# Kernel tuning notes

Hardware: AMD Instinct MI355X
Metric: run time of the kernel (lower is better)

## Reference

```python
import jax, jax.numpy as jnp
import numpy as np

B, C, H, W = 4, 128, 64, 64
CO = 128

def setup_inputs() -> dict:
    key = jax.random.key(0)
    ks = jax.random.split(key, 10)
    s = 1.0 / np.sqrt(C)
    return {
        "x":  jax.random.normal(ks[0], (B, C, H, W), dtype=jnp.float32),
        "Wq": jax.random.uniform(ks[1], (C, C), jnp.float32, -s, s),
        "bq": jax.random.uniform(ks[2], (C,), jnp.float32, -s, s),
        "Wk": jax.random.uniform(ks[3], (C, C), jnp.float32, -s, s),
        "bk": jax.random.uniform(ks[4], (C,), jnp.float32, -s, s),
        "Wv": jax.random.uniform(ks[5], (C, C), jnp.float32, -s, s),
        "bv": jax.random.uniform(ks[6], (C,), jnp.float32, -s, s),
        "gamma": jnp.ones((1,), dtype=jnp.float32),
        "Wo": jax.random.uniform(ks[7], (CO, C), jnp.float32, -s, s),
        "bo": jax.random.uniform(ks[8], (CO,), jnp.float32, -s, s),
    }

def reference(x, Wq, bq, Wk, bk, Wv, bv, gamma, Wo, bo):
    b, c, h, w = x.shape
    xf = x.reshape(b, c, h * w)                       # [B,C,N]
    # 1x1 convs == channel matmuls
    Q = jnp.einsum('oc,bcn->bon', Wq, xf) + bq[None, :, None]
    K = jnp.einsum('oc,bcn->bon', Wk, xf) + bk[None, :, None]
    V = jnp.einsum('oc,bcn->bon', Wv, xf) + bv[None, :, None]
    # attention[b,i,j] = softmax_j( sum_c Q[b,c,i] K[b,c,j] )  (unscaled)
    scores = jnp.einsum('bci,bcj->bij', Q, K)         # [B,N,N]
    attn = jax.nn.softmax(scores, axis=-1)
    # selfAtten[b,c,i] = sum_j V[b,c,j] attn[b,i,j]
    sa = jnp.einsum('bcj,bij->bci', V, attn)          # [B,C,N]
    sa = gamma[0] * sa + xf
    out = jnp.einsum('oc,bcn->bon', Wo, sa) + bo[None, :, None]
    return out.reshape(b, Wo.shape[0], h, w)
```

## Files before the change

### kernel.cpp

```cpp
#include <hip/hip_runtime.h>

#define BB 4
#define CC 128
#define NN 4096

typedef float f32x4 __attribute__((ext_vector_type(4)));
typedef __bf16 bf16x8 __attribute__((ext_vector_type(8)));

#define MFMA16(A, B, C) __builtin_amdgcn_mfma_f32_16x16x32_bf16((A), (B), (C), 0, 0, 0)

typedef __attribute__((address_space(3))) void lds_void;
typedef __attribute__((address_space(1))) void glob_void;
#define GLD16(g, l) __builtin_amdgcn_global_load_lds((const glob_void*)(g), (lds_void*)(l), 16, 0, 0)

__device__ __forceinline__ int fK(int r) { return (r & 3) | (((r >> 3) & 1) << 2); }

__global__ __launch_bounds__(256)
void pack_w(const float* __restrict__ Wq, const float* __restrict__ bq,
            const float* __restrict__ Wk, const float* __restrict__ bk,
            const float* __restrict__ Wv, const float* __restrict__ bv,
            const float* __restrict__ Wo, const float* __restrict__ bo,
            __bf16* __restrict__ Wpk, float* __restrict__ bpk)
{
    const int mat = blockIdx.x >> 3;
    const int p   = blockIdx.x & 7;
    const int tid = threadIdx.x;
    const int ks  = tid >> 6;
    const int lane = tid & 63;
    const int col = lane & 15;
    const int quad = lane >> 4;

    const float LOG2E = 1.44269504088896340736f;
    const float* W = (mat == 0) ? Wq : (mat == 1) ? Wk : (mat == 2) ? Wv : Wo;
    const float* bsrc = (mat == 0) ? bq : (mat == 1) ? bk : (mat == 2) ? bv : bo;
    const float scale = (mat == 0) ? LOG2E : 1.0f;

    const float* wr = W + (size_t)(p * 16 + col) * CC + ks * 32 + quad * 8;
    float4 f0 = *(const float4*)wr;
    float4 f1 = *(const float4*)(wr + 4);
    bf16x8 a;
    a[0]=(__bf16)(f0.x*scale); a[1]=(__bf16)(f0.y*scale);
    a[2]=(__bf16)(f0.z*scale); a[3]=(__bf16)(f0.w*scale);
    a[4]=(__bf16)(f1.x*scale); a[5]=(__bf16)(f1.y*scale);
    a[6]=(__bf16)(f1.z*scale); a[7]=(__bf16)(f1.w*scale);
    *(bf16x8*)&Wpk[(((size_t)(mat * 8 + p) * 4 + ks) * 64 + lane) * 8] = a;

    if (p == 0 && tid < 128) bpk[mat * 128 + tid] = bsrc[tid] * scale;
}

__global__ __launch_bounds__(256, 2)
void qkv_gemm(const float* __restrict__ x,
              const __bf16* __restrict__ Wpk, const float* __restrict__ bpk,
              __bf16* __restrict__ Qt, __bf16* __restrict__ Kt,
              __bf16* __restrict__ Vblk)
{
    const int b    = blockIdx.y;
    const int n0   = blockIdx.x * 64;
    const int tid  = threadIdx.x;
    const int lane = tid & 63;
    const int wv   = __builtin_amdgcn_readfirstlane(tid >> 6);
    const int col  = lane & 15;
    const int quad = lane >> 4;

    __shared__ __bf16 xs[64 * 144];
    __shared__ __bf16 vs[128 * 64];

    {
        const int n  = tid & 63;
        const int c0 = tid >> 6;
        const float* xb = x + ((size_t)b * CC) * NN + n0 + n;
#pragma unroll
        for (int i = 0; i < 16; i++) {
            int c = (c0 + i * 4) * 2;
            float v0 = xb[(size_t)c * NN];
            float v1 = xb[(size_t)(c + 1) * NN];
            union { __bf16 h[2]; unsigned u; } pk;
            pk.h[0] = (__bf16)v0; pk.h[1] = (__bf16)v1;
            *(unsigned*)&xs[n * 144 + c] = pk.u;
        }
    }
    __syncthreads();

    bf16x8 Bf[4][4];
#pragma unroll
    for (int ng = 0; ng < 4; ng++)
#pragma unroll
        for (int ks = 0; ks < 4; ks++)
            Bf[ng][ks] = *(const bf16x8*)&xs[(ng * 16 + col) * 144 + ks * 32 + quad * 8];

#pragma unroll 1
    for (int p = 0; p < 6; p++) {
        const int mat = p >> 1;
        const int pg  = wv + 4 * (p & 1);
        const int o0  = pg * 16;

        bf16x8 Af[4];
#pragma unroll
        for (int ks = 0; ks < 4; ks++)
            Af[ks] = *(const bf16x8*)&Wpk[(((size_t)(mat * 8 + pg) * 4 + ks) * 64 + lane) * 8];

        f32x4 D[4];
#pragma unroll
        for (int ng = 0; ng < 4; ng++) D[ng] = (f32x4){0.f, 0.f, 0.f, 0.f};
#pragma unroll
        for (int ks = 0; ks < 4; ks++)
#pragma unroll
            for (int ng = 0; ng < 4; ng++)
                D[ng] = MFMA16(Af[ks], Bf[ng][ks], D[ng]);

        float4 bias = *(const float4*)(bpk + mat * 128 + o0 + quad * 4);

#pragma unroll
        for (int ng = 0; ng < 4; ng++) {
            const int n = ng * 16 + col;
            float v[4];
#pragma unroll
            for (int r = 0; r < 4; r++)
                v[r] = D[ng][r] + ((const float*)&bias)[r];
            if (mat == 0) {
                union { __bf16 h[4]; uint2 u; } pk;
                for (int r = 0; r < 4; r++) pk.h[r] = (__bf16)v[r];
                *(uint2*)&Qt[((size_t)b * NN + n0 + n) * CC + o0 + quad * 4] = pk.u;
            } else if (mat == 1) {
                const int chunk = ((o0 + quad * 4) >> 3) ^ fK(n);
                union { __bf16 h[4]; uint2 u; } pk;
                for (int r = 0; r < 4; r++) pk.h[r] = (__bf16)v[r];
                *(uint2*)&Kt[((size_t)b * NN + n0 + n) * CC + chunk * 8 + (quad & 1) * 4] = pk.u;
            } else {
#pragma unroll
                for (int r = 0; r < 4; r++)
                    vs[(o0 + quad * 4 + r) * 64 + n] = (__bf16)v[r];
            }
        }
    }
    __syncthreads();

    {
        __bf16* vd = Vblk + (((size_t)b * 64 + (n0 >> 6)) * CC) * 64;
#pragma unroll
        for (int e = 0; e < 4; e++) {
            int idx = e * 256 + tid;
            int c = idx >> 3, ch = idx & 7;
            bf16x8 v = *(const bf16x8*)&vs[c * 64 + ch * 8];
            *(bf16x8*)&vd[c * 64 + ((ch ^ (c & 7)) * 8)] = v;
        }
    }
}

__global__ __launch_bounds__(256, 2)
void flash_attn(const __bf16* __restrict__ Qt, const __bf16* __restrict__ Kt,
                const __bf16* __restrict__ Vblk,
                float* __restrict__ Opart, float* __restrict__ Lpart)
{
    const int blk = blockIdx.x;
    const int b   = blk & 3;
    const int jhi = (blk >> 2) & 1;
    const int rr  = blk >> 3;
    const int js  = jhi * 2 + (rr & 1);
    const int i0  = (rr >> 1) * 128;

    const int tid  = threadIdx.x;
    const int lane = tid & 63;
    const int iw   = __builtin_amdgcn_readfirstlane(tid >> 6);
    const int col  = lane & 15;
    const int quad = lane >> 4;

    __shared__ __align__(16) char smem[69632];
    char* Kbytes = smem;
    char* Vbytes = smem + 16384;
    __bf16* Vh = (__bf16*)Vbytes;

#pragma unroll
    for (int e = 0; e < 4; e++) {
        int k = e * 256 + tid;
        Vh[128 * 64 + k] = (__bf16)((k < 64) ? 1.0f : 0.0f);
    }

    const __bf16* Qb = Qt + (size_t)b * NN * CC;
    const char*   Ks = (const char*)(Kt + (size_t)b * NN * CC);
    const char*   Vs = (const char*)(Vblk + ((size_t)b * 64 * CC) * 64);

    const int ibase = i0 + iw * 32;

    bf16x8 qf[2][4];
#pragma unroll
    for (int ig = 0; ig < 2; ig++)
#pragma unroll
        for (int ks = 0; ks < 4; ks++)
            qf[ig][ks] = *(const bf16x8*)(Qb + (size_t)(ibase + ig * 16 + col) * CC
                                             + ks * 32 + quad * 8);

    const int perm = ((col & 12) << 1) | (col & 3);
    const int fR   = fK(perm);
    int kaddr[4][4];
    const int joff[4] = {0, 4, 32, 36};
#pragma unroll
    for (int jg = 0; jg < 4; jg++)
#pragma unroll
        for (int ks = 0; ks < 4; ks++)
            kaddr[jg][ks] = (perm + joff[jg]) * 256 + (((ks * 4 + quad) ^ fR) * 16);
    int vaddr[8][2], oaddr[2];
#pragma unroll
    for (int cg = 0; cg < 8; cg++)
#pragma unroll
        for (int t = 0; t < 2; t++)
            vaddr[cg][t] = (cg * 16 + col) * 128 + (((t * 4 + quad) ^ (col & 7)) * 16);
#pragma unroll
    for (int t = 0; t < 2; t++)
        oaddr[t] = (128 + col) * 128 + (t * 4 + quad) * 16;

    f32x4 O[2][8], lacc[2];
#pragma unroll
    for (int ig = 0; ig < 2; ig++) {
#pragma unroll
        for (int cg = 0; cg < 8; cg++) O[ig][cg] = (f32x4){0.f, 0.f, 0.f, 0.f};
        lacc[ig] = (f32x4){0.f, 0.f, 0.f, 0.f};
    }

#pragma unroll 1
    for (int t16 = 0; t16 < 16; t16++) {
        const int jt = js * 16 + t16;
        const char* kg = Ks + (size_t)jt * 16384;
        const char* vg = Vs + (size_t)jt * 16384;
#pragma unroll
        for (int q = 0; q < 4; q++) {
            const int call = iw * 4 + q;
            GLD16(kg + call * 1024 + lane * 16, Kbytes + call * 1024 + lane * 16);
            GLD16(vg + call * 1024 + lane * 16, Vbytes + call * 1024 + lane * 16);
        }
        __syncthreads();

        f32x4 S[2][4];
#pragma unroll
        for (int ig = 0; ig < 2; ig++)
#pragma unroll
            for (int jg = 0; jg < 4; jg++)
                S[ig][jg] = (f32x4){-32.f, -32.f, -32.f, -32.f};
#pragma unroll
        for (int ks = 0; ks < 4; ks++) {
            bf16x8 k0 = *(const bf16x8*)(Kbytes + kaddr[0][ks]);
            bf16x8 k1 = *(const bf16x8*)(Kbytes + kaddr[1][ks]);
            bf16x8 k2 = *(const bf16x8*)(Kbytes + kaddr[2][ks]);
            bf16x8 k3 = *(const bf16x8*)(Kbytes + kaddr[3][ks]);
            S[0][0] = MFMA16(k0, qf[0][ks], S[0][0]);
            S[1][0] = MFMA16(k0, qf[1][ks], S[1][0]);
            S[0][1] = MFMA16(k1, qf[0][ks], S[0][1]);
            S[1][1] = MFMA16(k1, qf[1][ks], S[1][1]);
            S[0][2] = MFMA16(k2, qf[0][ks], S[0][2]);
            S[1][2] = MFMA16(k2, qf[1][ks], S[1][2]);
            S[0][3] = MFMA16(k3, qf[0][ks], S[0][3]);
            S[1][3] = MFMA16(k3, qf[1][ks], S[1][3]);
        }

#pragma unroll
        for (int ig = 0; ig < 2; ig++)
#pragma unroll
            for (int jg = 0; jg < 4; jg++)
#pragma unroll
                for (int r = 0; r < 4; r++)
                    S[ig][jg][r] = __builtin_amdgcn_exp2f(S[ig][jg][r]);

#pragma unroll
        for (int t = 0; t < 2; t++) {
            bf16x8 pf0, pf1;
#pragma unroll
            for (int e = 0; e < 8; e++) {
                int jg = 2 * t + (e >> 2), r = e & 3;
                pf0[e] = (__bf16)S[0][jg][r];
                pf1[e] = (__bf16)S[1][jg][r];
            }
#pragma unroll
            for (int cg = 0; cg < 8; cg++) {
                bf16x8 vf = *(const bf16x8*)(Vbytes + vaddr[cg][t]);
                O[0][cg] = MFMA16(vf, pf0, O[0][cg]);
                O[1][cg] = MFMA16(vf, pf1, O[1][cg]);
            }
            bf16x8 of = *(const bf16x8*)(Vbytes + oaddr[t]);
            lacc[0] = MFMA16(of, pf0, lacc[0]);
            lacc[1] = MFMA16(of, pf1, lacc[1]);
        }
        __syncthreads();
    }

    float* Ol = (float*)smem;
    float* Ll = (float*)(smem + 67584);
#pragma unroll
    for (int ig = 0; ig < 2; ig++) {
#pragma unroll
        for (int cg = 0; cg < 8; cg++)
#pragma unroll
            for (int r = 0; r < 4; r++)
                Ol[(cg * 16 + quad * 4 + r) * 132 + iw * 32 + ig * 16 + col] = O[ig][cg][r];
        if (quad == 0) Ll[iw * 32 + ig * 16 + col] = lacc[ig][0];
    }
    __syncthreads();
    {
        float* Od = Opart + (((size_t)b * 4 + js) * CC) * NN + i0;
#pragma unroll
        for (int e = 0; e < 16; e++) {
            int k = e * 256 + tid;
            int c = k >> 5, i4 = (k & 31) * 4;
            float4 v = *(const float4*)(Ol + c * 132 + i4);
            *(float4*)(Od + (size_t)c * NN + i4) = v;
        }
        if (tid < 128)
            Lpart[((size_t)b * 4 + js) * NN + i0 + tid] = Ll[tid];
    }
}

__global__ __launch_bounds__(256, 2)
void proj_out(const float* __restrict__ Opart, const float* __restrict__ Lpart,
              const float* __restrict__ x,
              const __bf16* __restrict__ Wpk, const float* __restrict__ bpk,
              const float* __restrict__ gamma, float* __restrict__ out)
{
    const int b    = blockIdx.y;
    const int n0   = blockIdx.x * 64;
    const int tid  = threadIdx.x;
    const int lane = tid & 63;
    const int wv   = __builtin_amdgcn_readfirstlane(tid >> 6);
    const int col  = lane & 15;
    const int quad = lane >> 4;

    __shared__ __bf16 sas[64 * 144];
    __shared__ float  outs[128 * 66];

    const float g = gamma[0];

    {
        const int n  = tid & 63;
        const int c0 = tid >> 6;
        const size_t nb = (size_t)b * 4;
        float l = Lpart[(nb + 0) * NN + n0 + n] + Lpart[(nb + 1) * NN + n0 + n]
                + Lpart[(nb + 2) * NN + n0 + n] + Lpart[(nb + 3) * NN + n0 + n];
        const float gl = g / l;
        const float* xb = x + ((size_t)b * CC) * NN + n0 + n;
        const float* Ob = Opart + (nb * CC) * NN + n0 + n;
#pragma unroll
        for (int i = 0; i < 16; i++) {
            int c = (c0 + i * 4) * 2;
            float s0 = 0.f, s1 = 0.f;
#pragma unroll
            for (int jsp = 0; jsp < 4; jsp++) {
                s0 += Ob[((size_t)jsp * CC + c) * NN];
                s1 += Ob[((size_t)jsp * CC + c + 1) * NN];
            }
            float v0 = xb[(size_t)c * NN] + s0 * gl;
            float v1 = xb[(size_t)(c + 1) * NN] + s1 * gl;
            union { __bf16 h[2]; unsigned u; } pk;
            pk.h[0] = (__bf16)v0; pk.h[1] = (__bf16)v1;
            *(unsigned*)&sas[n * 144 + c] = pk.u;
        }
    }
    __syncthreads();

    bf16x8 Bf[4][4];
#pragma unroll
    for (int ng = 0; ng < 4; ng++)
#pragma unroll
        for (int ks = 0; ks < 4; ks++)
            Bf[ng][ks] = *(const bf16x8*)&sas[(ng * 16 + col) * 144 + ks * 32 + quad * 8];

#pragma unroll
    for (int p = 0; p < 2; p++) {
        const int pg = wv * 2 + p;
        const int o0 = pg * 16;
        bf16x8 Af[4];
#pragma unroll
        for (int ks = 0; ks < 4; ks++)
            Af[ks] = *(const bf16x8*)&Wpk[(((size_t)(3 * 8 + pg) * 4 + ks) * 64 + lane) * 8];

        f32x4 D[4];
#pragma unroll
        for (int ng = 0; ng < 4; ng++) D[ng] = (f32x4){0.f, 0.f, 0.f, 0.f};
#pragma unroll
        for (int ks = 0; ks < 4; ks++)
#pragma unroll
            for (int ng = 0; ng < 4; ng++)
                D[ng] = MFMA16(Af[ks], Bf[ng][ks], D[ng]);

        float4 bias = *(const float4*)(bpk + 3 * 128 + o0 + quad * 4);
#pragma unroll
        for (int ng = 0; ng < 4; ng++)
#pragma unroll
            for (int r = 0; r < 4; r++)
                outs[(o0 + quad * 4 + r) * 66 + ng * 16 + col]
                    = D[ng][r] + ((const float*)&bias)[r];
    }
    __syncthreads();

    {
        float* od = out + ((size_t)b * CC) * NN + n0;
#pragma unroll
        for (int e = 0; e < 32; e++) {
            int k = e * 256 + tid;
            int o = k >> 6, n = k & 63;
            od[(size_t)o * NN + n] = outs[o * 66 + n];
        }
    }
}

extern "C" void kernel_launch(void* const* d_in, const int* in_sizes, int n_in,
                              void* d_out, int out_size, void* d_ws, size_t ws_size,
                              hipStream_t stream)
{
    const float* x  = (const float*)d_in[0];
    const float* Wq = (const float*)d_in[1];
    const float* bq = (const float*)d_in[2];
    const float* Wk = (const float*)d_in[3];
    const float* bk = (const float*)d_in[4];
    const float* Wv = (const float*)d_in[5];
    const float* bv = (const float*)d_in[6];
    const float* gm = (const float*)d_in[7];
    const float* Wo = (const float*)d_in[8];
    const float* bo = (const float*)d_in[9];

    __bf16* Qt    = (__bf16*)d_ws;
    __bf16* Kt    = Qt + (size_t)BB * NN * CC;
    __bf16* Vblk  = Kt + (size_t)BB * NN * CC;
    float*  Opart = (float*)(Vblk + (size_t)BB * NN * CC);
    float*  Lpart = Opart + (size_t)16 * CC * NN;
    __bf16* Wpk   = (__bf16*)(Lpart + (size_t)16 * NN);
    float*  bpk   = (float*)(Wpk + 4 * 8 * 4 * 64 * 8);
    float*  out   = (float*)d_out;

    pack_w<<<32, 256, 0, stream>>>(Wq, bq, Wk, bk, Wv, bv, Wo, bo, Wpk, bpk);
    qkv_gemm<<<dim3(64, 4), 256, 0, stream>>>(x, Wpk, bpk, Qt, Kt, Vblk);
    flash_attn<<<512, 256, 0, stream>>>(Qt, Kt, Vblk, Opart, Lpart);
    proj_out<<<dim3(64, 4), 256, 0, stream>>>(Opart, Lpart, x, Wpk, bpk, gm, out);
}
```

Baseline: 132.3 us.

## Double key-split factor and halve GEMM tiles to raise parallelism

Flash attention now splits the key dimension into 8 partitions instead of 4, launching 1024 blocks with half the key tiles each. Its shared memory drops to about 34 KB and launch bounds are raised to 3 blocks per CU. Partial outputs are written directly to global memory rather than staged through LDS, and the QKV and output-projection kernels use 32-column tiles to double their grid sizes. The aim is better CU occupancy and load balance, at the cost of twice the partial-output traffic and more reduction work in proj_out.

```diff
diff --git a/kernel.cpp b/kernel.cpp
--- a/kernel.cpp
+++ b/kernel.cpp
@@ -55,23 +55,23 @@
               __bf16* __restrict__ Vblk)
 {
     const int b    = blockIdx.y;
-    const int n0   = blockIdx.x * 64;
+    const int n0   = blockIdx.x * 32;
     const int tid  = threadIdx.x;
     const int lane = tid & 63;
     const int wv   = __builtin_amdgcn_readfirstlane(tid >> 6);
     const int col  = lane & 15;
     const int quad = lane >> 4;
 
-    __shared__ __bf16 xs[64 * 144];
-    __shared__ __bf16 vs[128 * 64];
+    __shared__ __bf16 xs[32 * 144];
+    __shared__ __bf16 vs[128 * 32];
 
     {
-        const int n  = tid & 63;
-        const int c0 = tid >> 6;
+        const int n  = tid & 31;
+        const int c0 = tid >> 5;
         const float* xb = x + ((size_t)b * CC) * NN + n0 + n;
 #pragma unroll
-        for (int i = 0; i < 16; i++) {
-            int c = (c0 + i * 4) * 2;
+        for (int i = 0; i < 8; i++) {
+            int c = (c0 + i * 8) * 2;
             float v0 = xb[(size_t)c * NN];
             float v1 = xb[(size_t)(c + 1) * NN];
             union { __bf16 h[2]; unsigned u; } pk;
@@ -81,9 +81,9 @@
     }
     __syncthreads();
 
-    bf16x8 Bf[4][4];
-#pragma unroll
-    for (int ng = 0; ng < 4; ng++)
+    bf16x8 Bf[2][4];
+#pragma unroll
+    for (int ng = 0; ng < 2; ng++)
 #pragma unroll
         for (int ks = 0; ks < 4; ks++)
             Bf[ng][ks] = *(const bf16x8*)&xs[(ng * 16 + col) * 144 + ks * 32 + quad * 8];
@@ -99,19 +99,19 @@
         for (int ks = 0; ks < 4; ks++)
             Af[ks] = *(const bf16x8*)&Wpk[(((size_t)(mat * 8 + pg) * 4 + ks) * 64 + lane) * 8];
 
-        f32x4 D[4];
-#pragma unroll
-        for (int ng = 0; ng < 4; ng++) D[ng] = (f32x4){0.f, 0.f, 0.f, 0.f};
-#pragma unroll
-        for (int ks = 0; ks < 4; ks++)
-#pragma unroll
-            for (int ng = 0; ng < 4; ng++)
+        f32x4 D[2];
+#pragma unroll
+        for (int ng = 0; ng < 2; ng++) D[ng] = (f32x4){0.f, 0.f, 0.f, 0.f};
+#pragma unroll
+        for (int ks = 0; ks < 4; ks++)
+#pragma unroll
+            for (int ng = 0; ng < 2; ng++)
                 D[ng] = MFMA16(Af[ks], Bf[ng][ks], D[ng]);
 
         float4 bias = *(const float4*)(bpk + mat * 128 + o0 + quad * 4);
 
 #pragma unroll
-        for (int ng = 0; ng < 4; ng++) {
+        for (int ng = 0; ng < 2; ng++) {
             const int n = ng * 16 + col;
             float v[4];
 #pragma unroll
@@ -122,14 +122,15 @@
                 for (int r = 0; r < 4; r++) pk.h[r] = (__bf16)v[r];
                 *(uint2*)&Qt[((size_t)b * NN + n0 + n) * CC + o0 + quad * 4] = pk.u;
             } else if (mat == 1) {
-                const int chunk = ((o0 + quad * 4) >> 3) ^ fK(n);
+                const int rin = ((n0 & 32) + n) & 63;
+                const int chunk = ((o0 + quad * 4) >> 3) ^ fK(rin);
                 union { __bf16 h[4]; uint2 u; } pk;
                 for (int r = 0; r < 4; r++) pk.h[r] = (__bf16)v[r];
                 *(uint2*)&Kt[((size_t)b * NN + n0 + n) * CC + chunk * 8 + (quad & 1) * 4] = pk.u;
             } else {
 #pragma unroll
                 for (int r = 0; r < 4; r++)
-                    vs[(o0 + quad * 4 + r) * 64 + n] = (__bf16)v[r];
+                    vs[(o0 + quad * 4 + r) * 32 + n] = (__bf16)v[r];
             }
         }
     }
@@ -137,27 +138,29 @@
 
     {
         __bf16* vd = Vblk + (((size_t)b * 64 + (n0 >> 6)) * CC) * 64;
-#pragma unroll
-        for (int e = 0; e < 4; e++) {
+        const int chbase = (n0 & 32) >> 3;
+#pragma unroll
+        for (int e = 0; e < 2; e++) {
             int idx = e * 256 + tid;
-            int c = idx >> 3, ch = idx & 7;
-            bf16x8 v = *(const bf16x8*)&vs[c * 64 + ch * 8];
-            *(bf16x8*)&vd[c * 64 + ((ch ^ (c & 7)) * 8)] = v;
+            int c = idx >> 2, chl = idx & 3;
+            bf16x8 v = *(const bf16x8*)&vs[c * 32 + chl * 8];
+            *(bf16x8*)&vd[c * 64 + (((chbase + chl) ^ (c & 7)) * 8)] = v;
         }
     }
 }
 
-__global__ __launch_bounds__(256, 2)
+__global__ __launch_bounds__(256, 3)
 void flash_attn(const __bf16* __restrict__ Qt, const __bf16* __restrict__ Kt,
                 const __bf16* __restrict__ Vblk,
                 float* __restrict__ Opart, float* __restrict__ Lpart)
 {
     const int blk = blockIdx.x;
-    const int b   = blk & 3;
-    const int jhi = (blk >> 2) & 1;
-    const int rr  = blk >> 3;
-    const int js  = jhi * 2 + (rr & 1);
-    const int i0  = (rr >> 1) * 128;
+    const int b    = blk & 3;
+    const int jlow = (blk >> 2) & 1;
+    const int jhigh = (blk >> 3) & 3;
+    const int it32  = blk >> 5;
+    const int js   = (jhigh << 1) | jlow;
+    const int i0   = it32 * 128;
 
     const int tid  = threadIdx.x;
     const int lane = tid & 63;
@@ -165,7 +168,7 @@
     const int col  = lane & 15;
     const int quad = lane >> 4;
 
-    __shared__ __align__(16) char smem[69632];
+    __shared__ __align__(16) char smem[34816];
     char* Kbytes = smem;
     char* Vbytes = smem + 16384;
     __bf16* Vh = (__bf16*)Vbytes;
@@ -218,8 +221,8 @@
     }
 
 #pragma unroll 1
-    for (int t16 = 0; t16 < 16; t16++) {
-        const int jt = js * 16 + t16;
+    for (int t8 = 0; t8 < 8; t8++) {
+        const int jt = js * 8 + t8;
         const char* kg = Ks + (size_t)jt * 16384;
         const char* vg = Vs + (size_t)jt * 16384;
 #pragma unroll
@@ -282,29 +285,22 @@
         __syncthreads();
     }
 
-    float* Ol = (float*)smem;
-    float* Ll = (float*)(smem + 67584);
-#pragma unroll
-    for (int ig = 0; ig < 2; ig++) {
-#pragma unroll
-        for (int cg = 0; cg < 8; cg++)
-#pragma unroll
-            for (int r = 0; r < 4; r++)
-                Ol[(cg * 16 + quad * 4 + r) * 132 + iw * 32 + ig * 16 + col] = O[ig][cg][r];
-        if (quad == 0) Ll[iw * 32 + ig * 16 + col] = lacc[ig][0];
-    }
-    __syncthreads();
     {
-        float* Od = Opart + (((size_t)b * 4 + js) * CC) * NN + i0;
-#pragma unroll
-        for (int e = 0; e < 16; e++) {
-            int k = e * 256 + tid;
-            int c = k >> 5, i4 = (k & 31) * 4;
-            float4 v = *(const float4*)(Ol + c * 132 + i4);
-            *(float4*)(Od + (size_t)c * NN + i4) = v;
-        }
-        if (tid < 128)
-            Lpart[((size_t)b * 4 + js) * NN + i0 + tid] = Ll[tid];
+        float* Od = Opart + (((size_t)b * 8 + js) * CC) * NN + ibase;
+#pragma unroll
+        for (int ig = 0; ig < 2; ig++)
+#pragma unroll
+            for (int cg = 0; cg < 8; cg++)
+#pragma unroll
+                for (int r = 0; r < 4; r++)
+                    Od[(size_t)(cg * 16 + quad * 4 + r) * NN + ig * 16 + col]
+                        = O[ig][cg][r];
+        if (quad == 0) {
+            float* Ld = Lpart + ((size_t)b * 8 + js) * NN + ibase;
+#pragma unroll
+            for (int ig = 0; ig < 2; ig++)
+                Ld[ig * 16 + col] = lacc[ig][0];
+        }
     }
 }
 
@@ -315,33 +311,35 @@
               const float* __restrict__ gamma, float* __restrict__ out)
 {
     const int b    = blockIdx.y;
-    const int n0   = blockIdx.x * 64;
+    const int n0   = blockIdx.x * 32;
     const int tid  = threadIdx.x;
     const int lane = tid & 63;
     const int wv   = __builtin_amdgcn_readfirstlane(tid >> 6);
     const int col  = lane & 15;
     const int quad = lane >> 4;
 
-    __shared__ __bf16 sas[64 * 144];
-    __shared__ float  outs[128 * 66];
+    __shared__ __bf16 sas[32 * 144];
+    __shared__ float  outs[128 * 34];
 
     const float g = gamma[0];
 
     {
-        const int n  = tid & 63;
-        const int c0 = tid >> 6;
-        const size_t nb = (size_t)b * 4;
-        float l = Lpart[(nb + 0) * NN + n0 + n] + Lpart[(nb + 1) * NN + n0 + n]
-                + Lpart[(nb + 2) * NN + n0 + n] + Lpart[(nb + 3) * NN + n0 + n];
+        const int n  = tid & 31;
+        const int c0 = tid >> 5;
+        const size_t nb = (size_t)b * 8;
+        float l = 0.f;
+#pragma unroll
+        for (int jsp = 0; jsp < 8; jsp++)
+            l += Lpart[(nb + jsp) * NN + n0 + n];
         const float gl = g / l;
         const float* xb = x + ((size_t)b * CC) * NN + n0 + n;
         const float* Ob = Opart + (nb * CC) * NN + n0 + n;
 #pragma unroll
-        for (int i = 0; i < 16; i++) {
-            int c = (c0 + i * 4) * 2;
+        for (int i = 0; i < 8; i++) {
+            int c = (c0 + i * 8) * 2;
             float s0 = 0.f, s1 = 0.f;
 #pragma unroll
-            for (int jsp = 0; jsp < 4; jsp++) {
+            for (int jsp = 0; jsp < 8; jsp++) {
                 s0 += Ob[((size_t)jsp * CC + c) * NN];
                 s1 += Ob[((size_t)jsp * CC + c + 1) * NN];
             }
@@ -354,9 +352,9 @@
     }
     __syncthreads();
 
-    bf16x8 Bf[4][4];
-#pragma unroll
-    for (int ng = 0; ng < 4; ng++)
+    bf16x8 Bf[2][4];
+#pragma unroll
+    for (int ng = 0; ng < 2; ng++)
 #pragma unroll
         for (int ks = 0; ks < 4; ks++)
             Bf[ng][ks] = *(const bf16x8*)&sas[(ng * 16 + col) * 144 + ks * 32 + quad * 8];
@@ -370,21 +368,21 @@
         for (int ks = 0; ks < 4; ks++)
             Af[ks] = *(const bf16x8*)&Wpk[(((size_t)(3 * 8 + pg) * 4 + ks) * 64 + lane) * 8];
 
-        f32x4 D[4];
-#pragma unroll
-        for (int ng = 0; ng < 4; ng++) D[ng] = (f32x4){0.f, 0.f, 0.f, 0.f};
-#pragma unroll
-        for (int ks = 0; ks < 4; ks++)
-#pragma unroll
-            for (int ng = 0; ng < 4; ng++)
+        f32x4 D[2];
+#pragma unroll
+        for (int ng = 0; ng < 2; ng++) D[ng] = (f32x4){0.f, 0.f, 0.f, 0.f};
+#pragma unroll
+        for (int ks = 0; ks < 4; ks++)
+#pragma unroll
+            for (int ng = 0; ng < 2; ng++)
                 D[ng] = MFMA16(Af[ks], Bf[ng][ks], D[ng]);
 
         float4 bias = *(const float4*)(bpk + 3 * 128 + o0 + quad * 4);
 #pragma unroll
-        for (int ng = 0; ng < 4; ng++)
+        for (int ng = 0; ng < 2; ng++)
 #pragma unroll
             for (int r = 0; r < 4; r++)
-                outs[(o0 + quad * 4 + r) * 66 + ng * 16 + col]
+                outs[(o0 + quad * 4 + r) * 34 + ng * 16 + col]
                     = D[ng][r] + ((const float*)&bias)[r];
     }
     __syncthreads();
@@ -392,10 +390,10 @@
     {
         float* od = out + ((size_t)b * CC) * NN + n0;
 #pragma unroll
-        for (int e = 0; e < 32; e++) {
+        for (int e = 0; e < 16; e++) {
             int k = e * 256 + tid;
-            int o = k >> 6, n = k & 63;
-            od[(size_t)o * NN + n] = outs[o * 66 + n];
+            int o = k >> 5, n = k & 31;
+            od[(size_t)o * NN + n] = outs[o * 34 + n];
         }
     }
 }
@@ -419,13 +417,13 @@
     __bf16* Kt    = Qt + (size_t)BB * NN * CC;
     __bf16* Vblk  = Kt + (size_t)BB * NN * CC;
     float*  Opart = (float*)(Vblk + (size_t)BB * NN * CC);
-    float*  Lpart = Opart + (size_t)16 * CC * NN;
-    __bf16* Wpk   = (__bf16*)(Lpart + (size_t)16 * NN);
+    float*  Lpart = Opart + (size_t)32 * CC * NN;
+    __bf16* Wpk   = (__bf16*)(Lpart + (size_t)32 * NN);
     float*  bpk   = (float*)(Wpk + 4 * 8 * 4 * 64 * 8);
     float*  out   = (float*)d_out;
 
     pack_w<<<32, 256, 0, stream>>>(Wq, bq, Wk, bk, Wv, bv, Wo, bo, Wpk, bpk);
-    qkv_gemm<<<dim3(64, 4), 256, 0, stream>>>(x, Wpk, bpk, Qt, Kt, Vblk);
-    flash_attn<<<512, 256, 0, stream>>>(Qt, Kt, Vblk, Opart, Lpart);
-    proj_out<<<dim3(64, 4), 256, 0, stream>>>(Opart, Lpart, x, Wpk, bpk, gm, out);
+    qkv_gemm<<<dim3(128, 4), 256, 0, stream>>>(x, Wpk, bpk, Qt, Kt, Vblk);
+    flash_attn<<<1024, 256, 0, stream>>>(Qt, Kt, Vblk, Opart, Lpart);
+    proj_out<<<dim3(128, 4), 256, 0, stream>>>(Opart, Lpart, x, Wpk, bpk, gm, out);
 }
```

Result: slower. 145.9 us (+10.2%).

## Fuse attention with output projection and double-buffer K/V tiles

Applied to the files above, without the earlier changes.

The separate flash attention and projection kernels are merged into one. Each block now owns 64 query rows over the full key range, with two wave pairs splitting the key columns and combining partial O and row sums in LDS. This removes the Opart/Lpart partial-sum round trip through global memory and one kernel launch. K/V tiles are double-buffered so the next tile's loads overlap compute. The costs are halving the grid to 256 blocks, a longer serial loop per block, and output stores that go straight from MFMA fragments to global memory instead of being staged in LDS.

```diff
diff --git a/kernel.cpp b/kernel.cpp
--- a/kernel.cpp
+++ b/kernel.cpp
@@ -148,32 +148,32 @@
 }
 
 __global__ __launch_bounds__(256, 2)
-void flash_attn(const __bf16* __restrict__ Qt, const __bf16* __restrict__ Kt,
-                const __bf16* __restrict__ Vblk,
-                float* __restrict__ Opart, float* __restrict__ Lpart)
+void attn_fused(const __bf16* __restrict__ Qt, const __bf16* __restrict__ Kt,
+                const __bf16* __restrict__ Vblk, const float* __restrict__ x,
+                const __bf16* __restrict__ Wpk, const float* __restrict__ bpk,
+                const float* __restrict__ gamma, float* __restrict__ out)
 {
     const int blk = blockIdx.x;
     const int b   = blk & 3;
-    const int jhi = (blk >> 2) & 1;
-    const int rr  = blk >> 3;
-    const int js  = jhi * 2 + (rr & 1);
-    const int i0  = (rr >> 1) * 128;
+    const int it  = blk >> 2;
+    const int i0  = it * 64;
 
     const int tid  = threadIdx.x;
     const int lane = tid & 63;
-    const int iw   = __builtin_amdgcn_readfirstlane(tid >> 6);
+    const int wv   = __builtin_amdgcn_readfirstlane(tid >> 6);
+    const int iw   = wv & 1;
+    const int jw   = wv >> 1;
     const int col  = lane & 15;
     const int quad = lane >> 4;
 
     __shared__ __align__(16) char smem[69632];
-    char* Kbytes = smem;
-    char* Vbytes = smem + 16384;
-    __bf16* Vh = (__bf16*)Vbytes;
-
-#pragma unroll
-    for (int e = 0; e < 4; e++) {
+    __shared__ float lbuf[64];
+
+#pragma unroll
+    for (int e = 0; e < 8; e++) {
         int k = e * 256 + tid;
-        Vh[128 * 64 + k] = (__bf16)((k < 64) ? 1.0f : 0.0f);
+        __bf16* Vh = (__bf16*)(smem + (k >> 10) * 34816 + 16384);
+        Vh[8192 + (k & 1023)] = (__bf16)(((k & 1023) < 64) ? 1.0f : 0.0f);
     }
 
     const __bf16* Qb = Qt + (size_t)b * NN * CC;
@@ -181,7 +181,6 @@
     const char*   Vs = (const char*)(Vblk + ((size_t)b * 64 * CC) * 64);
 
     const int ibase = i0 + iw * 32;
-
     bf16x8 qf[2][4];
 #pragma unroll
     for (int ig = 0; ig < 2; ig++)
@@ -192,22 +191,17 @@
 
     const int perm = ((col & 12) << 1) | (col & 3);
     const int fR   = fK(perm);
-    int kaddr[4][4];
-    const int joff[4] = {0, 4, 32, 36};
-#pragma unroll
-    for (int jg = 0; jg < 4; jg++)
-#pragma unroll
-        for (int ks = 0; ks < 4; ks++)
-            kaddr[jg][ks] = (perm + joff[jg]) * 256 + (((ks * 4 + quad) ^ fR) * 16);
-    int vaddr[8][2], oaddr[2];
+    int kaddr[2][4];
+#pragma unroll
+    for (int g = 0; g < 2; g++)
+#pragma unroll
+        for (int ks = 0; ks < 4; ks++)
+            kaddr[g][ks] = (perm + jw * 32 + 4 * g) * 256 + (((ks * 4 + quad) ^ fR) * 16);
+    int vaddr[8];
 #pragma unroll
     for (int cg = 0; cg < 8; cg++)
-#pragma unroll
-        for (int t = 0; t < 2; t++)
-            vaddr[cg][t] = (cg * 16 + col) * 128 + (((t * 4 + quad) ^ (col & 7)) * 16);
-#pragma unroll
-    for (int t = 0; t < 2; t++)
-        oaddr[t] = (128 + col) * 128 + (t * 4 + quad) * 16;
+        vaddr[cg] = (cg * 16 + col) * 128 + (((jw * 4 + quad) ^ (col & 7)) * 16);
+    const int oaddr = (128 + col) * 128 + (jw * 4 + quad) * 16;
 
     f32x4 O[2][8], lacc[2];
 #pragma unroll
@@ -217,139 +211,120 @@
         lacc[ig] = (f32x4){0.f, 0.f, 0.f, 0.f};
     }
 
+#pragma unroll
+    for (int q = 0; q < 4; q++) {
+        const int call = wv * 4 + q;
+        GLD16(Ks + call * 1024 + lane * 16, smem + call * 1024 + lane * 16);
+        GLD16(Vs + call * 1024 + lane * 16, smem + 16384 + call * 1024 + lane * 16);
+    }
+
 #pragma unroll 1
-    for (int t16 = 0; t16 < 16; t16++) {
-        const int jt = js * 16 + t16;
-        const char* kg = Ks + (size_t)jt * 16384;
-        const char* vg = Vs + (size_t)jt * 16384;
-#pragma unroll
-        for (int q = 0; q < 4; q++) {
-            const int call = iw * 4 + q;
-            GLD16(kg + call * 1024 + lane * 16, Kbytes + call * 1024 + lane * 16);
-            GLD16(vg + call * 1024 + lane * 16, Vbytes + call * 1024 + lane * 16);
-        }
+    for (int t = 0; t < 64; t++) {
         __syncthreads();
 
-        f32x4 S[2][4];
+        char* Kb = smem + (t & 1) * 34816;
+        char* Vb = Kb + 16384;
+
+        if (t < 63) {
+            const char* kg = Ks + (size_t)(t + 1) * 16384;
+            const char* vg = Vs + (size_t)(t + 1) * 16384;
+            char* kd = smem + ((t + 1) & 1) * 34816;
+#pragma unroll
+            for (int q = 0; q < 4; q++) {
+                const int call = wv * 4 + q;
+                GLD16(kg + call * 1024 + lane * 16, kd + call * 1024 + lane * 16);
+                GLD16(vg + call * 1024 + lane * 16, kd + 16384 + call * 1024 + lane * 16);
+            }
+        }
+
+        f32x4 S[2][2];
 #pragma unroll
         for (int ig = 0; ig < 2; ig++)
 #pragma unroll
-            for (int jg = 0; jg < 4; jg++)
-                S[ig][jg] = (f32x4){-32.f, -32.f, -32.f, -32.f};
+            for (int g = 0; g < 2; g++)
+                S[ig][g] = (f32x4){-32.f, -32.f, -32.f, -32.f};
 #pragma unroll
         for (int ks = 0; ks < 4; ks++) {
-            bf16x8 k0 = *(const bf16x8*)(Kbytes + kaddr[0][ks]);
-            bf16x8 k1 = *(const bf16x8*)(Kbytes + kaddr[1][ks]);
-            bf16x8 k2 = *(const bf16x8*)(Kbytes + kaddr[2][ks]);
-            bf16x8 k3 = *(const bf16x8*)(Kbytes + kaddr[3][ks]);
+            bf16x8 k0 = *(const bf16x8*)(Kb + kaddr[0][ks]);
+            bf16x8 k1 = *(const bf16x8*)(Kb + kaddr[1][ks]);
             S[0][0] = MFMA16(k0, qf[0][ks], S[0][0]);
             S[1][0] = MFMA16(k0, qf[1][ks], S[1][0]);
             S[0][1] = MFMA16(k1, qf[0][ks], S[0][1]);
             S[1][1] = MFMA16(k1, qf[1][ks], S[1][1]);
-            S[0][2] = MFMA16(k2, qf[0][ks], S[0][2]);
-            S[1][2] = MFMA16(k2, qf[1][ks], S[1][2]);
-            S[0][3] = MFMA16(k3, qf[0][ks], S[0][3]);
-            S[1][3] = MFMA16(k3, qf[1][ks], S[1][3]);
         }
 
 #pragma unroll
         for (int ig = 0; ig < 2; ig++)
 #pragma unroll
-            for (int jg = 0; jg < 4; jg++)
+            for (int g = 0; g < 2; g++)
 #pragma unroll
                 for (int r = 0; r < 4; r++)
-                    S[ig][jg][r] = __builtin_amdgcn_exp2f(S[ig][jg][r]);
-
-#pragma unroll
-        for (int t = 0; t < 2; t++) {
-            bf16x8 pf0, pf1;
-#pragma unroll
-            for (int e = 0; e < 8; e++) {
-                int jg = 2 * t + (e >> 2), r = e & 3;
-                pf0[e] = (__bf16)S[0][jg][r];
-                pf1[e] = (__bf16)S[1][jg][r];
-            }
-#pragma unroll
-            for (int cg = 0; cg < 8; cg++) {
-                bf16x8 vf = *(const bf16x8*)(Vbytes + vaddr[cg][t]);
-                O[0][cg] = MFMA16(vf, pf0, O[0][cg]);
-                O[1][cg] = MFMA16(vf, pf1, O[1][cg]);
-            }
-            bf16x8 of = *(const bf16x8*)(Vbytes + oaddr[t]);
-            lacc[0] = MFMA16(of, pf0, lacc[0]);
-            lacc[1] = MFMA16(of, pf1, lacc[1]);
-        }
-        __syncthreads();
-    }
-
-    float* Ol = (float*)smem;
-    float* Ll = (float*)(smem + 67584);
-#pragma unroll
-    for (int ig = 0; ig < 2; ig++) {
-#pragma unroll
-        for (int cg = 0; cg < 8; cg++)
-#pragma unroll
-            for (int r = 0; r < 4; r++)
-                Ol[(cg * 16 + quad * 4 + r) * 132 + iw * 32 + ig * 16 + col] = O[ig][cg][r];
-        if (quad == 0) Ll[iw * 32 + ig * 16 + col] = lacc[ig][0];
-    }
-    __syncthreads();
+                    S[ig][g][r] = __builtin_amdgcn_exp2f(S[ig][g][r]);
+
+        bf16x8 pf[2];
+#pragma unroll
+        for (int ig = 0; ig < 2; ig++) {
+            bf16x8 pa;
+#pragma unroll
+            for (int e = 0; e < 8; e++)
+                pa[e] = (__bf16)S[ig][e >> 2][e & 3];
+            pf[ig] = pa;
+        }
+#pragma unroll
+        for (int cg = 0; cg < 8; cg++) {
+            bf16x8 vf = *(const bf16x8*)(Vb + vaddr[cg]);
+            O[0][cg] = MFMA16(vf, pf[0], O[0][cg]);
+            O[1][cg] = MFMA16(vf, pf[1], O[1][cg]);
+        }
+        {
+            bf16x8 of = *(const bf16x8*)(Vb + oaddr);
+            lacc[0] = MFMA16(of, pf[0], lacc[0]);
+            lacc[1] = MFMA16(of, pf[1], lacc[1]);
+        }
+    }
+    __syncthreads();
+
+    float* Om = (float*)smem;
+    if (jw == 0) {
+#pragma unroll
+        for (int ig = 0; ig < 2; ig++) {
+#pragma unroll
+            for (int cg = 0; cg < 8; cg++)
+#pragma unroll
+                for (int r = 0; r < 4; r++)
+                    Om[(cg * 16 + quad * 4 + r) * 66 + iw * 32 + ig * 16 + col] = O[ig][cg][r];
+            if (quad == 0) lbuf[iw * 32 + ig * 16 + col] = lacc[ig][0];
+        }
+    }
+    __syncthreads();
+    if (jw == 1) {
+#pragma unroll
+        for (int ig = 0; ig < 2; ig++) {
+#pragma unroll
+            for (int cg = 0; cg < 8; cg++)
+#pragma unroll
+                for (int r = 0; r < 4; r++)
+                    Om[(cg * 16 + quad * 4 + r) * 66 + iw * 32 + ig * 16 + col] += O[ig][cg][r];
+            if (quad == 0) lbuf[iw * 32 + ig * 16 + col] += lacc[ig][0];
+        }
+    }
+    __syncthreads();
+
+    __bf16* sas = (__bf16*)(smem + 34816);
     {
-        float* Od = Opart + (((size_t)b * 4 + js) * CC) * NN + i0;
-#pragma unroll
-        for (int e = 0; e < 16; e++) {
-            int k = e * 256 + tid;
-            int c = k >> 5, i4 = (k & 31) * 4;
-            float4 v = *(const float4*)(Ol + c * 132 + i4);
-            *(float4*)(Od + (size_t)c * NN + i4) = v;
-        }
-        if (tid < 128)
-            Lpart[((size_t)b * 4 + js) * NN + i0 + tid] = Ll[tid];
-    }
-}
-
-__global__ __launch_bounds__(256, 2)
-void proj_out(const float* __restrict__ Opart, const float* __restrict__ Lpart,
-              const float* __restrict__ x,
-              const __bf16* __restrict__ Wpk, const float* __restrict__ bpk,
-              const float* __restrict__ gamma, float* __restrict__ out)
-{
-    const int b    = blockIdx.y;
-    const int n0   = blockIdx.x * 64;
-    const int tid  = threadIdx.x;
-    const int lane = tid & 63;
-    const int wv   = __builtin_amdgcn_readfirstlane(tid >> 6);
-    const int col  = lane & 15;
-    const int quad = lane >> 4;
-
-    __shared__ __bf16 sas[64 * 144];
-    __shared__ float  outs[128 * 66];
-
-    const float g = gamma[0];
-
-    {
-        const int n  = tid & 63;
+        const float g = gamma[0];
+        const int i  = tid & 63;
         const int c0 = tid >> 6;
-        const size_t nb = (size_t)b * 4;
-        float l = Lpart[(nb + 0) * NN + n0 + n] + Lpart[(nb + 1) * NN + n0 + n]
-                + Lpart[(nb + 2) * NN + n0 + n] + Lpart[(nb + 3) * NN + n0 + n];
-        const float gl = g / l;
-        const float* xb = x + ((size_t)b * CC) * NN + n0 + n;
-        const float* Ob = Opart + (nb * CC) * NN + n0 + n;
-#pragma unroll
-        for (int i = 0; i < 16; i++) {
-            int c = (c0 + i * 4) * 2;
-            float s0 = 0.f, s1 = 0.f;
-#pragma unroll
-            for (int jsp = 0; jsp < 4; jsp++) {
-                s0 += Ob[((size_t)jsp * CC + c) * NN];
-                s1 += Ob[((size_t)jsp * CC + c + 1) * NN];
-            }
-            float v0 = xb[(size_t)c * NN] + s0 * gl;
-            float v1 = xb[(size_t)(c + 1) * NN] + s1 * gl;
+        const float gl = g / lbuf[i];
+        const float* xb = x + ((size_t)b * CC) * NN + i0 + i;
+#pragma unroll
+        for (int kk = 0; kk < 16; kk++) {
+            int c = c0 * 32 + kk * 2;
+            float v0 = Om[c * 66 + i] * gl + xb[(size_t)c * NN];
+            float v1 = Om[(c + 1) * 66 + i] * gl + xb[(size_t)(c + 1) * NN];
             union { __bf16 h[2]; unsigned u; } pk;
             pk.h[0] = (__bf16)v0; pk.h[1] = (__bf16)v1;
-            *(unsigned*)&sas[n * 144 + c] = pk.u;
+            *(unsigned*)&sas[i * 136 + c] = pk.u;
         }
     }
     __syncthreads();
@@ -359,7 +334,7 @@
     for (int ng = 0; ng < 4; ng++)
 #pragma unroll
         for (int ks = 0; ks < 4; ks++)
-            Bf[ng][ks] = *(const bf16x8*)&sas[(ng * 16 + col) * 144 + ks * 32 + quad * 8];
+            Bf[ng][ks] = *(const bf16x8*)&sas[(ng * 16 + col) * 136 + ks * 32 + quad * 8];
 
 #pragma unroll
     for (int p = 0; p < 2; p++) {
@@ -384,19 +359,8 @@
         for (int ng = 0; ng < 4; ng++)
 #pragma unroll
             for (int r = 0; r < 4; r++)
-                outs[(o0 + quad * 4 + r) * 66 + ng * 16 + col]
+                out[((size_t)b * CC + o0 + quad * 4 + r) * NN + i0 + ng * 16 + col]
                     = D[ng][r] + ((const float*)&bias)[r];
-    }
-    __syncthreads();
-
-    {
-        float* od = out + ((size_t)b * CC) * NN + n0;
-#pragma unroll
-        for (int e = 0; e < 32; e++) {
-            int k = e * 256 + tid;
-            int o = k >> 6, n = k & 63;
-            od[(size_t)o * NN + n] = outs[o * 66 + n];
-        }
     }
 }
 
@@ -415,17 +379,14 @@
     const float* Wo = (const float*)d_in[8];
     const float* bo = (const float*)d_in[9];
 
-    __bf16* Qt    = (__bf16*)d_ws;
-    __bf16* Kt    = Qt + (size_t)BB * NN * CC;
-    __bf16* Vblk  = Kt + (size_t)BB * NN * CC;
-    float*  Opart = (float*)(Vblk + (size_t)BB * NN * CC);
-    float*  Lpart = Opart + (size_t)16 * CC * NN;
-    __bf16* Wpk   = (__bf16*)(Lpart + (size_t)16 * NN);
-    float*  bpk   = (float*)(Wpk + 4 * 8 * 4 * 64 * 8);
-    float*  out   = (float*)d_out;
+    __bf16* Qt   = (__bf16*)d_ws;
+    __bf16* Kt   = Qt + (size_t)BB * NN * CC;
+    __bf16* Vblk = Kt + (size_t)BB * NN * CC;
+    __bf16* Wpk  = Vblk + (size_t)BB * NN * CC;
+    float*  bpk  = (float*)(Wpk + 4 * 8 * 4 * 64 * 8);
+    float*  out  = (float*)d_out;
 
     pack_w<<<32, 256, 0, stream>>>(Wq, bq, Wk, bk, Wv, bv, Wo, bo, Wpk, bpk);
     qkv_gemm<<<dim3(64, 4), 256, 0, stream>>>(x, Wpk, bpk, Qt, Kt, Vblk);
-    flash_attn<<<512, 256, 0, stream>>>(Qt, Kt, Vblk, Opart, Lpart);
-    proj_out<<<dim3(64, 4), 256, 0, stream>>>(Opart, Lpart, x, Wpk, bpk, gm, out);
+    attn_fused<<<256, 256, 0, stream>>>(Qt, Kt, Vblk, x, Wpk, bpk, gm, out);
 }
```

Result: slower. 174.2 us (+31.6%).
